# Kernel optimization log

Measured on AMD Instinct MI355X. Metric: run time of the kernel, lower is better.

Reference implementation:

```python
import jax, jax.numpy as jnp
import numpy as np

QUERY_DIM = 192
KEY_DIM = 64
DIM_OUT = 128
C = QUERY_DIM + KEY_DIM  # 256
N = 10000
E = 320000
M = 5000


def setup_inputs() -> dict:
    key = jax.random.key(0)
    ks = jax.random.split(key, 16)
    s = 1.0 / np.sqrt(C)
    inp = {
        "query": jax.random.normal(ks[0], (N, QUERY_DIM), jnp.float32),
        "key_idx": jax.random.randint(ks[1], (N,), 0, KEY_DIM),
        "edge_index": jax.random.randint(ks[2], (2, E), 0, N),
        "mask_idx": jnp.sort(jax.random.randint(ks[3], (M,), 0, N)),
        "Wq": jax.random.normal(ks[4], (C, C), jnp.float32) * s,
        "bq": jnp.zeros((C,), jnp.float32),
        "Wk": jax.random.normal(ks[5], (C, C), jnp.float32) * s,
        "bk": jnp.zeros((C,), jnp.float32),
        "Wv": jax.random.normal(ks[6], (C, C), jnp.float32) * s,
        "bv": jnp.zeros((C,), jnp.float32),
        "Ws": jax.random.normal(ks[7], (C, C), jnp.float32) * s,
        "bs": jnp.zeros((C,), jnp.float32),
        "Wo": jax.random.normal(ks[8], (KEY_DIM, DIM_OUT), jnp.float32) * (1.0 / np.sqrt(KEY_DIM)),
        "bo": jnp.zeros((DIM_OUT,), jnp.float32),
    }
    return inp


def reference(query, key_idx, edge_index, mask_idx, Wq, bq, Wk, bk, Wv, bv, Ws, bs, Wo, bo):
    # node features: [N, C] = concat(query, one_hot(key))
    x = jnp.concatenate([query, jax.nn.one_hot(key_idx, KEY_DIM, dtype=query.dtype)], axis=1)
    src, dst = edge_index[0], edge_index[1]  # messages flow src -> dst
    # node-level projections (dense GEMMs), then edge gather
    q_n = x @ Wq + bq
    k_n = x @ Wk + bk
    v_n = x @ Wv + bv
    q = q_n[dst]  # [E, C]
    k = k_n[src]
    v = v_n[src]
    score = jnp.sum(q * k, axis=-1) / jnp.sqrt(jnp.asarray(C, x.dtype))  # [E]
    # per-destination softmax over incoming edges
    m = jax.ops.segment_max(score, dst, num_segments=N)  # [N]
    m = jnp.where(jnp.isfinite(m), m, 0.0)
    e = jnp.exp(score - m[dst])
    denom = jax.ops.segment_sum(e, dst, num_segments=N)
    alpha = e / (denom[dst] + 1e-16)
    # scatter-aggregate weighted values + root/skip connection
    agg = jax.ops.segment_sum(alpha[:, None] * v, dst, num_segments=N)  # [N, C]
    out = agg + (x @ Ws + bs)
    h = jax.nn.relu(out[mask_idx])  # [M, C]
    h = h[:, QUERY_DIM:]  # [M, KEY_DIM]
    return h @ Wo + bo  # [M, DIM_OUT]
```

## Files before the change

### kernel.cpp

```cpp
#include <hip/hip_runtime.h>

#define QDIM 192
#define KDIM 64
#define CDIM 256
#define DOUT 128
#define CAPS 64
#define NVCOL 640
#define NEG_INF __int_as_float(0xFF800000)
#define LDP 200

typedef _Float16 hf2 __attribute__((ext_vector_type(2)));
typedef _Float16 half4 __attribute__((ext_vector_type(4)));
typedef _Float16 half8 __attribute__((ext_vector_type(8)));
typedef float floatx4 __attribute__((ext_vector_type(4)));

#if defined(__has_builtin)
#if __has_builtin(__builtin_amdgcn_fdot2)
#define HAVE_FDOT2 1
#endif
#endif

__device__ __forceinline__ hf2 bc_h2(unsigned u) { return __builtin_bit_cast(hf2, u); }

__device__ __forceinline__ float dot2acc(hf2 a, hf2 b, float c) {
#ifdef HAVE_FDOT2
    return __builtin_amdgcn_fdot2(a, b, c, false);
#else
    return c + (float)a[0] * (float)b[0] + (float)a[1] * (float)b[1];
#endif
}

__global__ __launch_bounds__(256) void prep_kernel(
        const float* __restrict__ query, _Float16* __restrict__ Qh,
        const float* __restrict__ Wq, const float* __restrict__ bq,
        const float* __restrict__ Wk, const float* __restrict__ bk,
        const float* __restrict__ Wv, const float* __restrict__ bv,
        const float* __restrict__ Ws, const float* __restrict__ bs,
        const int* __restrict__ mask, int M,
        _Float16* __restrict__ WhT, float* __restrict__ OB,
        int* __restrict__ deg4, int qchunks, int N) {
    int t = blockIdx.x * blockDim.x + threadIdx.x;
    if (t < qchunks) {
        float4 v = ((const float4*)query)[t];
        half4 h = { (_Float16)v.x, (_Float16)v.y, (_Float16)v.z, (_Float16)v.w };
        ((half4*)Qh)[t] = h;
        return;
    }
    t -= qchunks;
    if (t < NVCOL * QDIM) {
        int v = t / QDIM, r = t - v * QDIM;
        const float* Wseg; int col;
        if (v < 256)      { Wseg = Wq; col = v; }
        else if (v < 512) { Wseg = Wk; col = v - 256; }
        else if (v < 576) { Wseg = Wv; col = QDIM + (v - 512); }
        else              { Wseg = Ws; col = QDIM + (v - 576); }
        WhT[t] = (_Float16)Wseg[(size_t)r * CDIM + col];
        return;
    }
    t -= NVCOL * QDIM;
    if (t < NVCOL * KDIM) {
        int v = t >> 6, kidx = t & 63;
        const float* Wseg; const float* bseg; int col;
        if (v < 256)      { Wseg = Wq; bseg = bq; col = v; }
        else if (v < 512) { Wseg = Wk; bseg = bk; col = v - 256; }
        else if (v < 576) { Wseg = Wv; bseg = bv; col = QDIM + (v - 512); }
        else              { Wseg = Ws; bseg = bs; col = QDIM + (v - 576); }
        OB[t] = Wseg[(size_t)(QDIM + kidx) * CDIM + col] + bseg[col];
        return;
    }
    t -= NVCOL * KDIM;
    if (t < 4 * N) {
        int node = t >> 2;
        int lo = 0, hi = M;
        while (lo < hi) { int mid = (lo + hi) >> 1; if (mask[mid] < node) lo = mid + 1; else hi = mid; }
        bool found = (lo < M) && (mask[lo] == node);
        deg4[t] = found ? 0 : (int)0x80000000;
    }
}

__global__ __launch_bounds__(256) void gemm_nodes(
        const _Float16* __restrict__ Qh, const int* __restrict__ key_idx,
        const _Float16* __restrict__ WhT, const float* __restrict__ OB,
        const int* __restrict__ esrc, const int* __restrict__ edst,
        const int* __restrict__ mask, int M,
        int* deg4, int* __restrict__ adj, int E,
        _Float16* __restrict__ Qbuf, _Float16* __restrict__ Kbuf,
        _Float16* __restrict__ Vbuf, float* __restrict__ Sbuf, int N) {
    __shared__ __align__(16) _Float16 Bs[64 * LDP];
    int tid = threadIdx.x;
    int z = blockIdx.z;
    int bm = blockIdx.x * 64;

    bool doe[2] = {false, false};
    int srcv[2]; size_t ci[2] = {0, 0};
    if (z == 0) {
        int stride = gridDim.x * gridDim.y * 256;
        int base = (blockIdx.y * gridDim.x + blockIdx.x) * 256 + tid;
        #pragma unroll
        for (int q = 0; q < 2; q++) {
            int e = base + q * stride;
            if (e < E) {
                int d = edst[e];
                size_t c = (size_t)d * 4 + (e & 3);
                if (deg4[c] >= 0) {
                    doe[q] = true; srcv[q] = esrc[e]; ci[q] = c;
                }
            }
        }
    } else {
        if (bm >= M) return;
    }

    int bn = (z == 0) ? 256 + blockIdx.y * 64
                      : (blockIdx.y < 4 ? blockIdx.y * 64 : 576);

    int w = tid >> 6, l = tid & 63;
    int lrow = l & 15, quad = l >> 4;

    int ra = w * 16 + lrow;
    int gra = (z == 0) ? min(bm + ra, N - 1) : mask[min(bm + ra, M - 1)];
    const _Float16* abase = Qh + (size_t)gra * QDIM + quad * 8;
    half8 af[6];
    #pragma unroll
    for (int ks = 0; ks < 6; ks++) af[ks] = *(const half8*)(abase + ks * 32);

    #pragma unroll
    for (int it = 0; it < 6; it++) {
        int idx = tid + it * 256;
        int cc = idx / 24, q4 = idx % 24;
        uint4 vb = ((const uint4*)(WhT + (size_t)(bn + cc) * QDIM))[q4];
        *((uint4*)&Bs[cc * LDP + q4 * 8]) = vb;
    }
    __syncthreads();

    int slot[2] = {-1, -1};
    #pragma unroll
    for (int q = 0; q < 2; q++) if (doe[q]) slot[q] = atomicAdd(&deg4[ci[q]], 1);

    floatx4 acc[4] = {{0.f,0.f,0.f,0.f},{0.f,0.f,0.f,0.f},{0.f,0.f,0.f,0.f},{0.f,0.f,0.f,0.f}};
    #pragma unroll
    for (int ks = 0; ks < 6; ks++) {
        #pragma unroll
        for (int nt = 0; nt < 4; nt++) {
            half8 bf = *(const half8*)(&Bs[(nt * 16 + lrow) * LDP + quad * 8 + ks * 32]);
            acc[nt] = __builtin_amdgcn_mfma_f32_16x16x32_f16(af[ks], bf, acc[nt], 0, 0, 0);
        }
    }

    #pragma unroll
    for (int q = 0; q < 2; q++)
        if (doe[q] && (unsigned)slot[q] < CAPS) adj[ci[q] * CAPS + slot[q]] = srcv[q];

    int ki[4], grs[4];
    #pragma unroll
    for (int reg = 0; reg < 4; reg++) {
        int re = w * 16 + quad * 4 + reg;
        grs[reg] = (z == 0) ? min(bm + re, N - 1) : mask[min(bm + re, M - 1)];
        ki[reg] = key_idx[grs[reg]];
    }
    #pragma unroll
    for (int nt = 0; nt < 4; nt++) {
        int gc = bn + nt * 16 + lrow;
        const float* obc = OB + (size_t)gc * KDIM;
        #pragma unroll
        for (int reg = 0; reg < 4; reg++) {
            int gr = grs[reg];
            float v = acc[nt][reg] + obc[ki[reg]];
            if (gc < 256)      Qbuf[(size_t)gr * 256 + gc] = (_Float16)v;
            else if (gc < 512) Kbuf[(size_t)gr * 256 + (gc - 256)] = (_Float16)v;
            else if (gc < 576) Vbuf[(size_t)gr * KDIM + (gc - 512)] = (_Float16)v;
            else               Sbuf[(size_t)gr * KDIM + (gc - 576)] = v;
        }
    }
}

__global__ __launch_bounds__(256) void attend_out(
        const _Float16* __restrict__ Qbuf, const _Float16* __restrict__ Kbuf,
        const _Float16* __restrict__ Vbuf, const float* __restrict__ Sbuf,
        const int* __restrict__ deg4, const int* __restrict__ adj,
        const int* __restrict__ mask, const float* __restrict__ Wo,
        const float* __restrict__ bo, float* __restrict__ out, int M) {
    int w = threadIdx.x >> 6, lane = threadIdx.x & 63;
    int r = blockIdx.x * 4 + w;
    if (r >= M) return;
    int node = mask[r];
    if (r > 0 && mask[r - 1] == node) return;
    int l = lane & 15, g = lane >> 4;

    const uint4* qp = (const uint4*)(Qbuf + (size_t)node * 256 + l * 16);
    uint4 qa = qp[0], qb = qp[1];
    hf2 qh[8] = { bc_h2(qa.x), bc_h2(qa.y), bc_h2(qa.z), bc_h2(qa.w),
                  bc_h2(qb.x), bc_h2(qb.y), bc_h2(qb.z), bc_h2(qb.w) };

    int dn_g = min(deg4[(size_t)node * 4 + g], CAPS);
    int d0 = __shfl(dn_g, 0, 64), d1 = __shfl(dn_g, 16, 64);
    int d2 = __shfl(dn_g, 32, 64), d3 = __shfl(dn_g, 48, 64);
    int O1 = d0, O2 = d0 + d1, O3 = d0 + d1 + d2, T = O3 + d3;
    const size_t base4 = (size_t)node * 4 * CAPS;
    auto fs = [&](int j) -> int {
        int b = (j >= O1) + (j >= O2) + (j >= O3);
        int off = j - (b == 0 ? 0 : b == 1 ? O1 : b == 2 ? O2 : O3);
        return adj[base4 + (size_t)b * CAPS + off];
    };
    auto idxAt = [&](int p) -> int { return fs(min(g + 4 * p, T - 1)); };

    float m = NEG_INF, dsum = 0.f;
    float a0 = 0.f, a1 = 0.f, a2 = 0.f, a3 = 0.f;

    auto compute = [&](uint4 ka, uint4 kb, uint2 vv) {
        float d = 0.f;
        d = dot2acc(bc_h2(ka.x), qh[0], d);
        d = dot2acc(bc_h2(ka.y), qh[1], d);
        d = dot2acc(bc_h2(ka.z), qh[2], d);
        d = dot2acc(bc_h2(ka.w), qh[3], d);
        d = dot2acc(bc_h2(kb.x), qh[4], d);
        d = dot2acc(bc_h2(kb.y), qh[5], d);
        d = dot2acc(bc_h2(kb.z), qh[6], d);
        d = dot2acc(bc_h2(kb.w), qh[7], d);
        d += __shfl_xor(d, 1, 64);
        d += __shfl_xor(d, 2, 64);
        d += __shfl_xor(d, 4, 64);
        d += __shfl_xor(d, 8, 64);
        float sc = d * 0.0625f;
        float m_new = fmaxf(m, sc);
        float scale = __expf(m - m_new);
        float p = __expf(sc - m_new);
        dsum = dsum * scale + p;
        hf2 v01 = bc_h2(vv.x), v23 = bc_h2(vv.y);
        a0 = a0 * scale + p * (float)v01[0];
        a1 = a1 * scale + p * (float)v01[1];
        a2 = a2 * scale + p * (float)v23[0];
        a3 = a3 * scale + p * (float)v23[1];
        m = m_new;
    };

    int P = (g < T) ? ((T - g + 3) >> 2) : 0;
    uint4 kaA = {}, kbA = {}; uint2 vvA = {};
    uint4 kaB = {}, kbB = {}; uint2 vvB = {};
    int sC = 0, sD = 0;
    if (P > 0) {
        int sA = idxAt(0);
        const uint4* kp = (const uint4*)(Kbuf + (size_t)sA * 256 + l * 16);
        kaA = kp[0]; kbA = kp[1];
        vvA = *(const uint2*)(Vbuf + (size_t)sA * KDIM + l * 4);
        int sB = idxAt(1);
        const uint4* kp2 = (const uint4*)(Kbuf + (size_t)sB * 256 + l * 16);
        kaB = kp2[0]; kbB = kp2[1];
        vvB = *(const uint2*)(Vbuf + (size_t)sB * KDIM + l * 4);
        sC = idxAt(2); sD = idxAt(3);
    }
    for (int p = 0; p < P; p += 2) {
        compute(kaA, kbA, vvA);
        {
            const uint4* kp = (const uint4*)(Kbuf + (size_t)sC * 256 + l * 16);
            kaA = kp[0]; kbA = kp[1];
            vvA = *(const uint2*)(Vbuf + (size_t)sC * KDIM + l * 4);
        }
        int sC2 = idxAt(p + 4);
        if (p + 1 < P) compute(kaB, kbB, vvB);
        {
            const uint4* kp = (const uint4*)(Kbuf + (size_t)sD * 256 + l * 16);
            kaB = kp[0]; kbB = kp[1];
            vvB = *(const uint2*)(Vbuf + (size_t)sD * KDIM + l * 4);
        }
        int sD2 = idxAt(p + 5);
        sC = sC2; sD = sD2;
    }

    float Mx = fmaxf(m, __shfl_xor(m, 16, 64));
    Mx = fmaxf(Mx, __shfl_xor(Mx, 32, 64));
    float wgt = (m == NEG_INF) ? 0.f : __expf(m - Mx);
    float ds = dsum * wgt;
    ds += __shfl_xor(ds, 16, 64);
    ds += __shfl_xor(ds, 32, 64);
    a0 *= wgt; a1 *= wgt; a2 *= wgt; a3 *= wgt;
    a0 += __shfl_xor(a0, 16, 64); a0 += __shfl_xor(a0, 32, 64);
    a1 += __shfl_xor(a1, 16, 64); a1 += __shfl_xor(a1, 32, 64);
    a2 += __shfl_xor(a2, 16, 64); a2 += __shfl_xor(a2, 32, 64);
    a3 += __shfl_xor(a3, 16, 64); a3 += __shfl_xor(a3, 32, 64);
    float inv = 1.f / (ds + 1e-16f);

    float4 s4 = *((const float4*)(Sbuf + (size_t)node * KDIM + l * 4));
    float h0 = fmaxf(a0 * inv + s4.x, 0.f);
    float h1 = fmaxf(a1 * inv + s4.y, 0.f);
    float h2 = fmaxf(a2 * inv + s4.z, 0.f);
    float h3 = fmaxf(a3 * inv + s4.w, 0.f);

    float o0 = bo[lane], o1 = bo[lane + 64];
    #pragma unroll
    for (int c = 0; c < KDIM; c++) {
        float hc = (c & 3) == 0 ? h0 : (c & 3) == 1 ? h1 : (c & 3) == 2 ? h2 : h3;
        float hv = __shfl(hc, c >> 2, 64);
        o0 += hv * Wo[c * DOUT + lane];
        o1 += hv * Wo[c * DOUT + 64 + lane];
    }
    int rr = r;
    do {
        out[(size_t)rr * DOUT + lane] = o0;
        out[(size_t)rr * DOUT + 64 + lane] = o1;
        rr++;
    } while (rr < M && mask[rr] == node);
}

extern "C" void kernel_launch(void* const* d_in, const int* in_sizes, int n_in,
                              void* d_out, int out_size, void* d_ws, size_t ws_size,
                              hipStream_t stream) {
    const float* query    = (const float*)d_in[0];
    const int* key_idx    = (const int*)d_in[1];
    const int* edge_index = (const int*)d_in[2];
    const int* mask_idx   = (const int*)d_in[3];
    const float* Wq = (const float*)d_in[4];
    const float* bq = (const float*)d_in[5];
    const float* Wk = (const float*)d_in[6];
    const float* bk = (const float*)d_in[7];
    const float* Wv = (const float*)d_in[8];
    const float* bv = (const float*)d_in[9];
    const float* Ws = (const float*)d_in[10];
    const float* bs = (const float*)d_in[11];
    const float* Wo = (const float*)d_in[12];
    const float* bo = (const float*)d_in[13];

    int N = in_sizes[0] / QDIM;
    int E = in_sizes[2] / 2;
    int M = in_sizes[3];
    const int* esrc = edge_index;
    const int* edst = edge_index + E;

    char* wsb = (char*)d_ws;
    size_t off = 0;
    auto alloc = [&](size_t nbytes) { char* p = wsb + off; off += (nbytes + 15) & ~15ull; return p; };
    _Float16* Qh   = (_Float16*)alloc((size_t)N * QDIM * 2);
    _Float16* WhT  = (_Float16*)alloc((size_t)NVCOL * QDIM * 2);
    float* OB      = (float*)alloc((size_t)NVCOL * KDIM * 4);
    _Float16* Qbuf = (_Float16*)alloc((size_t)N * 256 * 2);
    _Float16* Kbuf = (_Float16*)alloc((size_t)N * 256 * 2);
    _Float16* Vbuf = (_Float16*)alloc((size_t)N * KDIM * 2);
    float* Sbuf    = (float*)alloc((size_t)N * KDIM * 4);
    int*   deg4    = (int*)alloc((size_t)N * 4 * 4);
    int*   adj     = (int*)alloc((size_t)N * 4 * CAPS * 4);

    int qchunks = N * QDIM / 4;
    int total1 = qchunks + NVCOL * QDIM + NVCOL * KDIM + 4 * N;
    prep_kernel<<<(total1 + 255) / 256, 256, 0, stream>>>(
        query, Qh, Wq, bq, Wk, bk, Wv, bv, Ws, bs, mask_idx, M, WhT, OB, deg4, qchunks, N);

    int xa = (N + 63) / 64, xm = (M + 63) / 64;
    dim3 ggrid((unsigned)max(xa, xm), 5, 2);
    gemm_nodes<<<ggrid, 256, 0, stream>>>(Qh, key_idx, WhT, OB, esrc, edst,
                                          mask_idx, M, deg4, adj, E,
                                          Qbuf, Kbuf, Vbuf, Sbuf, N);

    attend_out<<<(M + 3) / 4, 256, 0, stream>>>(Qbuf, Kbuf, Vbuf, Sbuf, deg4, adj,
                                                mask_idx, Wo, bo, (float*)d_out, M);
}
```

Measured before the change: 131.9 us.

## Fold Wk into query side: precompute Wq·Wkᵀ, score against raw source features

Uses q·k = x_dst Wq Wkᵀ x_srcᵀ: prep precomputes a fused 256x192 matrix so each masked destination gets a projected vector U, and the one-hot key part becomes a per-destination 64-entry lookup. The full K projection for all N nodes is dropped; instead the gather reads a packed per-source payload (raw fp16 query interleaved with V columns) plus the source's key index packed into the adjacency entry. This cuts the big N-row K GEMM and reduces gather bytes per edge, at the cost of a small O(256·192·256) weight product in prep and fp16 rounding of the fused matrix. The 3D grid is flattened into class-partitioned 1D blocks and edge bucketing is spread over three edges per thread.

```diff
diff --git a/kernel.cpp b/kernel.cpp
--- a/kernel.cpp
+++ b/kernel.cpp
@@ -5,7 +5,7 @@
 #define CDIM 256
 #define DOUT 128
 #define CAPS 64
-#define NVCOL 640
+#define NBCOL 384
 #define NEG_INF __int_as_float(0xFF800000)
 #define LDP 200
 
@@ -32,43 +32,72 @@
 
 __global__ __launch_bounds__(256) void prep_kernel(
         const float* __restrict__ query, _Float16* __restrict__ Qh,
+        _Float16* __restrict__ Pay,
         const float* __restrict__ Wq, const float* __restrict__ bq,
         const float* __restrict__ Wk, const float* __restrict__ bk,
         const float* __restrict__ Wv, const float* __restrict__ bv,
         const float* __restrict__ Ws, const float* __restrict__ bs,
         const int* __restrict__ mask, int M,
-        _Float16* __restrict__ WhT, float* __restrict__ OB,
+        _Float16* __restrict__ BhT, float* __restrict__ OBall,
         int* __restrict__ deg4, int qchunks, int N) {
     int t = blockIdx.x * blockDim.x + threadIdx.x;
     if (t < qchunks) {
         float4 v = ((const float4*)query)[t];
         half4 h = { (_Float16)v.x, (_Float16)v.y, (_Float16)v.z, (_Float16)v.w };
         ((half4*)Qh)[t] = h;
+        int h0 = t * 4;
+        int src = h0 / QDIM, i = h0 - src * QDIM;
+        *(half4*)(Pay + (size_t)src * 256 + (i / 12) * 16 + (i % 12)) = h;
         return;
     }
     t -= qchunks;
-    if (t < NVCOL * QDIM) {
-        int v = t / QDIM, r = t - v * QDIM;
-        const float* Wseg; int col;
-        if (v < 256)      { Wseg = Wq; col = v; }
-        else if (v < 512) { Wseg = Wk; col = v - 256; }
-        else if (v < 576) { Wseg = Wv; col = QDIM + (v - 512); }
-        else              { Wseg = Ws; col = QDIM + (v - 576); }
-        WhT[t] = (_Float16)Wseg[(size_t)r * CDIM + col];
-        return;
-    }
-    t -= NVCOL * QDIM;
-    if (t < NVCOL * KDIM) {
-        int v = t >> 6, kidx = t & 63;
+    if (t < 256 * QDIM) {
+        int j = t / QDIM, i = t - j * QDIM;
+        const float4* wq = (const float4*)(Wq + (size_t)i * CDIM);
+        const float4* wk = (const float4*)(Wk + (size_t)j * CDIM);
+        float acc = 0.f;
+        #pragma unroll 8
+        for (int c = 0; c < 64; c++) {
+            float4 a = wq[c], b = wk[c];
+            acc += a.x*b.x + a.y*b.y + a.z*b.z + a.w*b.w;
+        }
+        BhT[(size_t)j * QDIM + i] = (_Float16)acc;
+        return;
+    }
+    t -= 256 * QDIM;
+    if (t < 128 * QDIM) {
+        int c = t / QDIM, r = t - c * QDIM;
+        float val = (c < 64) ? Wv[(size_t)r * CDIM + QDIM + c]
+                             : Ws[(size_t)r * CDIM + QDIM + (c - 64)];
+        BhT[(size_t)(256 + c) * QDIM + r] = (_Float16)val;
+        return;
+    }
+    t -= 128 * QDIM;
+    if (t < 256 * KDIM) {
+        int j = t >> 6, ki = t & 63;
+        const float4* wk  = (const float4*)(Wk + (size_t)j * CDIM);
+        const float4* wq  = (const float4*)(Wq + (size_t)(QDIM + ki) * CDIM);
+        const float4* bqv = (const float4*)bq;
+        float acc = 0.f;
+        #pragma unroll 8
+        for (int c = 0; c < 64; c++) {
+            float4 b = wk[c], a = wq[c], q = bqv[c];
+            acc += b.x*(a.x+q.x) + b.y*(a.y+q.y) + b.z*(a.z+q.z) + b.w*(a.w+q.w);
+        }
+        OBall[(size_t)j * KDIM + ki] = acc;
+        return;
+    }
+    t -= 256 * KDIM;
+    if (t < 128 * KDIM) {
+        int jj = t >> 6, ki = t & 63;
         const float* Wseg; const float* bseg; int col;
-        if (v < 256)      { Wseg = Wq; bseg = bq; col = v; }
-        else if (v < 512) { Wseg = Wk; bseg = bk; col = v - 256; }
-        else if (v < 576) { Wseg = Wv; bseg = bv; col = QDIM + (v - 512); }
-        else              { Wseg = Ws; bseg = bs; col = QDIM + (v - 576); }
-        OB[t] = Wseg[(size_t)(QDIM + kidx) * CDIM + col] + bseg[col];
-        return;
-    }
-    t -= NVCOL * KDIM;
+        if (jj < 64) { Wseg = Wv; bseg = bv; col = QDIM + jj; }
+        else         { Wseg = Ws; bseg = bs; col = QDIM + (jj - 64); }
+        OBall[(size_t)(256 + jj) * KDIM + ki] =
+            Wseg[(size_t)(QDIM + ki) * CDIM + col] + bseg[col];
+        return;
+    }
+    t -= 128 * KDIM;
     if (t < 4 * N) {
         int node = t >> 2;
         int lo = 0, hi = M;
@@ -80,45 +109,47 @@
 
 __global__ __launch_bounds__(256) void gemm_nodes(
         const _Float16* __restrict__ Qh, const int* __restrict__ key_idx,
-        const _Float16* __restrict__ WhT, const float* __restrict__ OB,
+        const _Float16* __restrict__ BhT, const float* __restrict__ OBall,
         const int* __restrict__ esrc, const int* __restrict__ edst,
         const int* __restrict__ mask, int M,
         int* deg4, int* __restrict__ adj, int E,
-        _Float16* __restrict__ Qbuf, _Float16* __restrict__ Kbuf,
-        _Float16* __restrict__ Vbuf, float* __restrict__ Sbuf, int N) {
+        _Float16* __restrict__ Ubuf, _Float16* __restrict__ Pay,
+        float* __restrict__ Sbuf, int N, int XA, int XM) {
     __shared__ __align__(16) _Float16 Bs[64 * LDP];
     int tid = threadIdx.x;
-    int z = blockIdx.z;
-    int bm = blockIdx.x * 64;
-
-    bool doe[2] = {false, false};
-    int srcv[2]; size_t ci[2] = {0, 0};
-    if (z == 0) {
-        int stride = gridDim.x * gridDim.y * 256;
-        int base = (blockIdx.y * gridDim.x + blockIdx.x) * 256 + tid;
+    int b = blockIdx.x;
+    int cls, rb, bn;
+    if (b < XA)                 { cls = 0; rb = b;                bn = 256; }
+    else if (b < XA + 4 * XM)   { int u2 = b - XA; cls = 1; rb = u2 >> 2; bn = (u2 & 3) * 64; }
+    else                        { cls = 2; rb = b - XA - 4 * XM;  bn = 320; }
+    int bm = rb * 64;
+
+    bool doe[3] = {false, false, false};
+    int srcv[3]; size_t ci[3] = {0, 0, 0};
+    {
+        int stride = gridDim.x * 256;
+        int base = b * 256 + tid;
         #pragma unroll
-        for (int q = 0; q < 2; q++) {
+        for (int q = 0; q < 3; q++) {
             int e = base + q * stride;
             if (e < E) {
                 int d = edst[e];
                 size_t c = (size_t)d * 4 + (e & 3);
                 if (deg4[c] >= 0) {
-                    doe[q] = true; srcv[q] = esrc[e]; ci[q] = c;
+                    doe[q] = true;
+                    int s = esrc[e];
+                    srcv[q] = (s << 6) | (key_idx[s] & 63);
+                    ci[q] = c;
                 }
             }
         }
-    } else {
-        if (bm >= M) return;
-    }
-
-    int bn = (z == 0) ? 256 + blockIdx.y * 64
-                      : (blockIdx.y < 4 ? blockIdx.y * 64 : 576);
+    }
 
     int w = tid >> 6, l = tid & 63;
     int lrow = l & 15, quad = l >> 4;
 
     int ra = w * 16 + lrow;
-    int gra = (z == 0) ? min(bm + ra, N - 1) : mask[min(bm + ra, M - 1)];
+    int gra = (cls == 0) ? min(bm + ra, N - 1) : mask[min(bm + ra, M - 1)];
     const _Float16* abase = Qh + (size_t)gra * QDIM + quad * 8;
     half8 af[6];
     #pragma unroll
@@ -128,14 +159,14 @@
     for (int it = 0; it < 6; it++) {
         int idx = tid + it * 256;
         int cc = idx / 24, q4 = idx % 24;
-        uint4 vb = ((const uint4*)(WhT + (size_t)(bn + cc) * QDIM))[q4];
+        uint4 vb = ((const uint4*)(BhT + (size_t)(bn + cc) * QDIM))[q4];
         *((uint4*)&Bs[cc * LDP + q4 * 8]) = vb;
     }
     __syncthreads();
 
-    int slot[2] = {-1, -1};
-    #pragma unroll
-    for (int q = 0; q < 2; q++) if (doe[q]) slot[q] = atomicAdd(&deg4[ci[q]], 1);
+    int slot[3] = {-1, -1, -1};
+    #pragma unroll
+    for (int q = 0; q < 3; q++) if (doe[q]) slot[q] = atomicAdd(&deg4[ci[q]], 1);
 
     floatx4 acc[4] = {{0.f,0.f,0.f,0.f},{0.f,0.f,0.f,0.f},{0.f,0.f,0.f,0.f},{0.f,0.f,0.f,0.f}};
     #pragma unroll
@@ -148,35 +179,35 @@
     }
 
     #pragma unroll
-    for (int q = 0; q < 2; q++)
+    for (int q = 0; q < 3; q++)
         if (doe[q] && (unsigned)slot[q] < CAPS) adj[ci[q] * CAPS + slot[q]] = srcv[q];
 
     int ki[4], grs[4];
     #pragma unroll
     for (int reg = 0; reg < 4; reg++) {
         int re = w * 16 + quad * 4 + reg;
-        grs[reg] = (z == 0) ? min(bm + re, N - 1) : mask[min(bm + re, M - 1)];
+        grs[reg] = (cls == 0) ? min(bm + re, N - 1) : mask[min(bm + re, M - 1)];
         ki[reg] = key_idx[grs[reg]];
     }
     #pragma unroll
     for (int nt = 0; nt < 4; nt++) {
         int gc = bn + nt * 16 + lrow;
-        const float* obc = OB + (size_t)gc * KDIM;
+        const float* obc = OBall + (size_t)gc * KDIM;
         #pragma unroll
         for (int reg = 0; reg < 4; reg++) {
             int gr = grs[reg];
             float v = acc[nt][reg] + obc[ki[reg]];
-            if (gc < 256)      Qbuf[(size_t)gr * 256 + gc] = (_Float16)v;
-            else if (gc < 512) Kbuf[(size_t)gr * 256 + (gc - 256)] = (_Float16)v;
-            else if (gc < 576) Vbuf[(size_t)gr * KDIM + (gc - 512)] = (_Float16)v;
-            else               Sbuf[(size_t)gr * KDIM + (gc - 576)] = v;
+            if (gc < 256)      Ubuf[(size_t)gr * 256 + gc] = (_Float16)v;
+            else if (gc < 320) { int c = gc - 256;
+                                 Pay[(size_t)gr * 256 + (c >> 2) * 16 + 12 + (c & 3)] = (_Float16)v; }
+            else               Sbuf[(size_t)gr * KDIM + (gc - 320)] = v;
         }
     }
 }
 
 __global__ __launch_bounds__(256) void attend_out(
-        const _Float16* __restrict__ Qbuf, const _Float16* __restrict__ Kbuf,
-        const _Float16* __restrict__ Vbuf, const float* __restrict__ Sbuf,
+        const _Float16* __restrict__ Ubuf, const _Float16* __restrict__ Pay,
+        const float* __restrict__ Sbuf,
         const int* __restrict__ deg4, const int* __restrict__ adj,
         const int* __restrict__ mask, const float* __restrict__ Wo,
         const float* __restrict__ bo, float* __restrict__ out, int M) {
@@ -187,10 +218,11 @@
     if (r > 0 && mask[r - 1] == node) return;
     int l = lane & 15, g = lane >> 4;
 
-    const uint4* qp = (const uint4*)(Qbuf + (size_t)node * 256 + l * 16);
-    uint4 qa = qp[0], qb = qp[1];
-    hf2 qh[8] = { bc_h2(qa.x), bc_h2(qa.y), bc_h2(qa.z), bc_h2(qa.w),
-                  bc_h2(qb.x), bc_h2(qb.y), bc_h2(qb.z), bc_h2(qb.w) };
+    const uint2* up = (const uint2*)(Ubuf + (size_t)node * 256 + l * 12);
+    uint2 u0 = up[0], u1 = up[1], u2 = up[2];
+    hf2 uf[6] = { bc_h2(u0.x), bc_h2(u0.y), bc_h2(u1.x),
+                  bc_h2(u1.y), bc_h2(u2.x), bc_h2(u2.y) };
+    const _Float16* lutp = Ubuf + (size_t)node * 256 + QDIM;
 
     int dn_g = min(deg4[(size_t)node * 4 + g], CAPS);
     int d0 = __shfl(dn_g, 0, 64), d1 = __shfl(dn_g, 16, 64);
@@ -207,26 +239,24 @@
     float m = NEG_INF, dsum = 0.f;
     float a0 = 0.f, a1 = 0.f, a2 = 0.f, a3 = 0.f;
 
-    auto compute = [&](uint4 ka, uint4 kb, uint2 vv) {
+    auto compute = [&](uint4 A0, uint4 A1, float lut) {
         float d = 0.f;
-        d = dot2acc(bc_h2(ka.x), qh[0], d);
-        d = dot2acc(bc_h2(ka.y), qh[1], d);
-        d = dot2acc(bc_h2(ka.z), qh[2], d);
-        d = dot2acc(bc_h2(ka.w), qh[3], d);
-        d = dot2acc(bc_h2(kb.x), qh[4], d);
-        d = dot2acc(bc_h2(kb.y), qh[5], d);
-        d = dot2acc(bc_h2(kb.z), qh[6], d);
-        d = dot2acc(bc_h2(kb.w), qh[7], d);
+        d = dot2acc(bc_h2(A0.x), uf[0], d);
+        d = dot2acc(bc_h2(A0.y), uf[1], d);
+        d = dot2acc(bc_h2(A0.z), uf[2], d);
+        d = dot2acc(bc_h2(A0.w), uf[3], d);
+        d = dot2acc(bc_h2(A1.x), uf[4], d);
+        d = dot2acc(bc_h2(A1.y), uf[5], d);
         d += __shfl_xor(d, 1, 64);
         d += __shfl_xor(d, 2, 64);
         d += __shfl_xor(d, 4, 64);
         d += __shfl_xor(d, 8, 64);
-        float sc = d * 0.0625f;
+        float sc = (d + lut) * 0.0625f;
         float m_new = fmaxf(m, sc);
         float scale = __expf(m - m_new);
         float p = __expf(sc - m_new);
         dsum = dsum * scale + p;
-        hf2 v01 = bc_h2(vv.x), v23 = bc_h2(vv.y);
+        hf2 v01 = bc_h2(A1.z), v23 = bc_h2(A1.w);
         a0 = a0 * scale + p * (float)v01[0];
         a1 = a1 * scale + p * (float)v01[1];
         a2 = a2 * scale + p * (float)v23[0];
@@ -234,37 +264,37 @@
         m = m_new;
     };
 
-    int P = (g < T) ? ((T - g + 3) >> 2) : 0;
-    uint4 kaA = {}, kbA = {}; uint2 vvA = {};
-    uint4 kaB = {}, kbB = {}; uint2 vvB = {};
-    int sC = 0, sD = 0;
-    if (P > 0) {
-        int sA = idxAt(0);
-        const uint4* kp = (const uint4*)(Kbuf + (size_t)sA * 256 + l * 16);
-        kaA = kp[0]; kbA = kp[1];
-        vvA = *(const uint2*)(Vbuf + (size_t)sA * KDIM + l * 4);
-        int sB = idxAt(1);
-        const uint4* kp2 = (const uint4*)(Kbuf + (size_t)sB * 256 + l * 16);
-        kaB = kp2[0]; kbB = kp2[1];
-        vvB = *(const uint2*)(Vbuf + (size_t)sB * KDIM + l * 4);
-        sC = idxAt(2); sD = idxAt(3);
-    }
-    for (int p = 0; p < P; p += 2) {
-        compute(kaA, kbA, vvA);
+    int np = (g < T) ? ((T - g + 3) >> 2) : 0;
+    uint4 A0 = {}, A1 = {}, B0 = {}, B1 = {};
+    float lutA = 0.f, lutB = 0.f;
+    int vC = 0, vD = 0;
+    if (np > 0) {
+        int vA = idxAt(0);
+        const uint4* pp = (const uint4*)(Pay + (size_t)(vA >> 6) * 256 + l * 16);
+        A0 = pp[0]; A1 = pp[1];
+        lutA = (float)lutp[vA & 63];
+        int vB = idxAt(1);
+        const uint4* pb = (const uint4*)(Pay + (size_t)(vB >> 6) * 256 + l * 16);
+        B0 = pb[0]; B1 = pb[1];
+        lutB = (float)lutp[vB & 63];
+        vC = idxAt(2); vD = idxAt(3);
+    }
+    for (int p = 0; p < np; p += 2) {
+        compute(A0, A1, lutA);
         {
-            const uint4* kp = (const uint4*)(Kbuf + (size_t)sC * 256 + l * 16);
-            kaA = kp[0]; kbA = kp[1];
-            vvA = *(const uint2*)(Vbuf + (size_t)sC * KDIM + l * 4);
-        }
-        int sC2 = idxAt(p + 4);
-        if (p + 1 < P) compute(kaB, kbB, vvB);
+            const uint4* pp = (const uint4*)(Pay + (size_t)(vC >> 6) * 256 + l * 16);
+            A0 = pp[0]; A1 = pp[1];
+            lutA = (float)lutp[vC & 63];
+        }
+        int vC2 = idxAt(p + 4);
+        if (p + 1 < np) compute(B0, B1, lutB);
         {
-            const uint4* kp = (const uint4*)(Kbuf + (size_t)sD * 256 + l * 16);
-            kaB = kp[0]; kbB = kp[1];
-            vvB = *(const uint2*)(Vbuf + (size_t)sD * KDIM + l * 4);
-        }
-        int sD2 = idxAt(p + 5);
-        sC = sC2; sD = sD2;
+            const uint4* pb = (const uint4*)(Pay + (size_t)(vD >> 6) * 256 + l * 16);
+            B0 = pb[0]; B1 = pb[1];
+            lutB = (float)lutp[vD & 63];
+        }
+        int vD2 = idxAt(p + 5);
+        vC = vC2; vD = vD2;
     }
 
     float Mx = fmaxf(m, __shfl_xor(m, 16, 64));
@@ -319,6 +349,7 @@
     const float* bs = (const float*)d_in[11];
     const float* Wo = (const float*)d_in[12];
     const float* bo = (const float*)d_in[13];
+    (void)bk;
 
     int N = in_sizes[0] / QDIM;
     int E = in_sizes[2] / 2;
@@ -330,26 +361,26 @@
     size_t off = 0;
     auto alloc = [&](size_t nbytes) { char* p = wsb + off; off += (nbytes + 15) & ~15ull; return p; };
     _Float16* Qh   = (_Float16*)alloc((size_t)N * QDIM * 2);
-    _Float16* WhT  = (_Float16*)alloc((size_t)NVCOL * QDIM * 2);
-    float* OB      = (float*)alloc((size_t)NVCOL * KDIM * 4);
-    _Float16* Qbuf = (_Float16*)alloc((size_t)N * 256 * 2);
-    _Float16* Kbuf = (_Float16*)alloc((size_t)N * 256 * 2);
-    _Float16* Vbuf = (_Float16*)alloc((size_t)N * KDIM * 2);
+    _Float16* Pay  = (_Float16*)alloc((size_t)N * 256 * 2);
+    _Float16* Ubuf = (_Float16*)alloc((size_t)N * 256 * 2);
+    _Float16* BhT  = (_Float16*)alloc((size_t)NBCOL * QDIM * 2);
+    float* OBall   = (float*)alloc((size_t)NBCOL * KDIM * 4);
     float* Sbuf    = (float*)alloc((size_t)N * KDIM * 4);
     int*   deg4    = (int*)alloc((size_t)N * 4 * 4);
     int*   adj     = (int*)alloc((size_t)N * 4 * CAPS * 4);
 
     int qchunks = N * QDIM / 4;
-    int total1 = qchunks + NVCOL * QDIM + NVCOL * KDIM + 4 * N;
+    int total1 = qchunks + 256 * QDIM + 128 * QDIM + 256 * KDIM + 128 * KDIM + 4 * N;
     prep_kernel<<<(total1 + 255) / 256, 256, 0, stream>>>(
-        query, Qh, Wq, bq, Wk, bk, Wv, bv, Ws, bs, mask_idx, M, WhT, OB, deg4, qchunks, N);
-
-    int xa = (N + 63) / 64, xm = (M + 63) / 64;
-    dim3 ggrid((unsigned)max(xa, xm), 5, 2);
-    gemm_nodes<<<ggrid, 256, 0, stream>>>(Qh, key_idx, WhT, OB, esrc, edst,
-                                          mask_idx, M, deg4, adj, E,
-                                          Qbuf, Kbuf, Vbuf, Sbuf, N);
-
-    attend_out<<<(M + 3) / 4, 256, 0, stream>>>(Qbuf, Kbuf, Vbuf, Sbuf, deg4, adj,
+        query, Qh, Pay, Wq, bq, Wk, bk, Wv, bv, Ws, bs, mask_idx, M,
+        BhT, OBall, deg4, qchunks, N);
+
+    int XA = (N + 63) / 64, XM = (M + 63) / 64;
+    int NB = XA + 4 * XM + XM;
+    gemm_nodes<<<NB, 256, 0, stream>>>(Qh, key_idx, BhT, OBall, esrc, edst,
+                                       mask_idx, M, deg4, adj, E,
+                                       Ubuf, Pay, Sbuf, N, XA, XM);
+
+    attend_out<<<(M + 3) / 4, 256, 0, stream>>>(Ubuf, Pay, Sbuf, deg4, adj,
                                                 mask_idx, Wo, bo, (float*)d_out, M);
 }
```

Result: slower. 153.9 us (+16.7%).
